# Performance work log

Measured on AMD Instinct MI355X. Metric: run time of the kernel, lower is better.

Reference implementation:

```python
import jax, jax.numpy as jnp
import numpy as np

NUM_ATOMS = 4_000_000
NUM_TYPES = 11

def setup_inputs() -> dict:
    key = jax.random.key(0)
    k1, k2 = jax.random.split(key)
    input_coords = jax.random.normal(k1, (3 * NUM_ATOMS,), dtype=jnp.float32)
    atom_types = jax.random.randint(k2, (NUM_ATOMS,), 0, NUM_TYPES, dtype=jnp.int64)
    return {"input_coords": input_coords, "atom_types": atom_types, "num_atom_types": NUM_TYPES}

def reference(input_coords, atom_types, num_atom_types):
    # counts per atom type  [T]
    counts = jnp.bincount(atom_types, length=num_atom_types).astype(jnp.int32)
    # exclusive prefix sum -> bucket offsets  [T]
    offsets = (jnp.cumsum(counts) - counts).astype(jnp.int32)
    # stable sort by type reproduces the C++ bucket fill order:
    # atoms of the same type keep their original relative order.
    perm = jnp.argsort(atom_types, stable=True)  # [N] source index for each output slot
    coords3 = input_coords.reshape(-1, 3)        # [N,3]
    typed_coords = coords3[perm].reshape(-1)     # [3N] type-grouped flat coords
    return typed_coords, counts, offsets
```

## Files before the change

kernel.cpp:

```cpp
#include <hip/hip_runtime.h>

#define NTYPES 11
#define BLOCK  256
#define ITEMS  16
#define CHUNK  (BLOCK * ITEMS)

__global__ __launch_bounds__(BLOCK) void hist_kernel(
    const int* __restrict__ types, int N, int B, int* __restrict__ bc) {
  __shared__ int shCnt[NTYPES];
  const int tid = threadIdx.x;
  const int b = blockIdx.x;
  if (tid < NTYPES) shCnt[tid] = 0;
  __syncthreads();

  const int run = b * CHUNK + tid * ITEMS;
  int cnt[NTYPES];
#pragma unroll
  for (int t = 0; t < NTYPES; ++t) cnt[t] = 0;

  if (run < N) {
    const int4* p = (const int4*)(types + run);
    int4 a0 = p[0], a1 = p[1], a2 = p[2], a3 = p[3];
    int ty[ITEMS] = {a0.x, a0.y, a0.z, a0.w, a1.x, a1.y, a1.z, a1.w,
                     a2.x, a2.y, a2.z, a2.w, a3.x, a3.y, a3.z, a3.w};
#pragma unroll
    for (int k = 0; k < ITEMS; ++k) {
#pragma unroll
      for (int t = 0; t < NTYPES; ++t) cnt[t] += (ty[k] == t) ? 1 : 0;
    }
  }

  const int lane = tid & 63;
#pragma unroll
  for (int t = 0; t < NTYPES; ++t) {
    int v = cnt[t];
    for (int o = 32; o >= 1; o >>= 1) v += __shfl_down(v, o);
    if (lane == 0) atomicAdd(&shCnt[t], v);
  }
  __syncthreads();
  if (tid < NTYPES) bc[tid * B + b] = shCnt[tid];
}

__global__ __launch_bounds__(1024) void scan_kernel(
    const int* __restrict__ bc, int B, int* __restrict__ scanOut,
    int* __restrict__ offs, float* __restrict__ outTail) {
  __shared__ int wtot[16];
  __shared__ int totals[NTYPES];
  const int tid = threadIdx.x;
  const int lane = tid & 63;
  const int wave = tid >> 6;

  for (int t = 0; t < NTYPES; ++t) {
    const int x = (tid < B) ? bc[t * B + tid] : 0;
    int incl = x;
#pragma unroll
    for (int o = 1; o < 64; o <<= 1) {
      int v = __shfl_up(incl, o);
      if (lane >= o) incl += v;
    }
    if (lane == 63) wtot[wave] = incl;
    __syncthreads();
    if (wave == 0) {
      int y = (lane < 16) ? wtot[lane] : 0;
#pragma unroll
      for (int o = 1; o < 16; o <<= 1) {
        int v = __shfl_up(y, o);
        if (lane >= o) y += v;
      }
      if (lane < 16) wtot[lane] = y;
    }
    __syncthreads();
    incl += (wave > 0) ? wtot[wave - 1] : 0;
    if (tid < B) scanOut[t * B + tid] = incl - x;
    if (tid == 1023) totals[t] = incl;
    __syncthreads();
  }

  if (tid == 0) {
    int off = 0;
    for (int t = 0; t < NTYPES; ++t) {
      const int c = totals[t];
      offs[t] = off;
      outTail[t] = (float)c;
      outTail[NTYPES + t] = (float)off;
      off += c;
    }
  }
}

__global__ __launch_bounds__(BLOCK) void scatter_kernel(
    const float* __restrict__ coords, const int* __restrict__ types,
    const int* __restrict__ scanOut, const int* __restrict__ offs, int N,
    int B, float* __restrict__ out) {
  const int tid = threadIdx.x;
  const int b = blockIdx.x;
  const int lane = tid & 63;
  const int wave = tid >> 6;
  const int run = b * CHUNK + tid * ITEMS;
  const bool active = (run < N);

  int ty[ITEMS];
  int cnt[NTYPES];
#pragma unroll
  for (int t = 0; t < NTYPES; ++t) cnt[t] = 0;
#pragma unroll
  for (int k = 0; k < ITEMS; ++k) ty[k] = -1;

  if (active) {
    const int4* p = (const int4*)(types + run);
    int4 a0 = p[0], a1 = p[1], a2 = p[2], a3 = p[3];
    int tt[ITEMS] = {a0.x, a0.y, a0.z, a0.w, a1.x, a1.y, a1.z, a1.w,
                     a2.x, a2.y, a2.z, a2.w, a3.x, a3.y, a3.z, a3.w};
#pragma unroll
    for (int k = 0; k < ITEMS; ++k) ty[k] = tt[k];
#pragma unroll
    for (int k = 0; k < ITEMS; ++k) {
#pragma unroll
      for (int t = 0; t < NTYPES; ++t) cnt[t] += (ty[k] == t) ? 1 : 0;
    }
  }

  __shared__ int wtot[NTYPES][4];
  int rank[NTYPES];
#pragma unroll
  for (int t = 0; t < NTYPES; ++t) {
    int incl = cnt[t];
#pragma unroll
    for (int o = 1; o < 64; o <<= 1) {
      int v = __shfl_up(incl, o);
      if (lane >= o) incl += v;
    }
    if (lane == 63) wtot[t][wave] = incl;
    rank[t] = incl - cnt[t];
  }
  __syncthreads();
#pragma unroll
  for (int t = 0; t < NTYPES; ++t) {
    int wb = 0;
#pragma unroll
    for (int w = 0; w < 3; ++w) wb += (w < wave) ? wtot[t][w] : 0;
    rank[t] += wb + offs[t] + scanOut[t * B + b];
  }

  if (active) {
    const float4* cp = (const float4*)(coords + (size_t)run * 3);
    float c[ITEMS * 3];
#pragma unroll
    for (int q = 0; q < 12; ++q) {
      float4 v = cp[q];
      c[4 * q + 0] = v.x;
      c[4 * q + 1] = v.y;
      c[4 * q + 2] = v.z;
      c[4 * q + 3] = v.w;
    }
#pragma unroll
    for (int k = 0; k < ITEMS; ++k) {
      const int t0 = ty[k];
      int dst = 0;
#pragma unroll
      for (int t = 0; t < NTYPES; ++t) {
        if (t0 == t) {
          dst = rank[t];
          rank[t] += 1;
        }
      }
      out[3 * (size_t)dst + 0] = c[3 * k + 0];
      out[3 * (size_t)dst + 1] = c[3 * k + 1];
      out[3 * (size_t)dst + 2] = c[3 * k + 2];
    }
  }
}

extern "C" void kernel_launch(void* const* d_in, const int* in_sizes, int n_in,
                              void* d_out, int out_size, void* d_ws,
                              size_t ws_size, hipStream_t stream) {
  const float* coords = (const float*)d_in[0];
  const int* types = (const int*)d_in[1];
  const int N = in_sizes[1];
  const int B = (N + CHUNK - 1) / CHUNK;

  int* bc = (int*)d_ws;
  int* scanOut = bc + NTYPES * B;
  int* offs = scanOut + NTYPES * B;
  float* out = (float*)d_out;
  float* outTail = out + (size_t)3 * N;

  hist_kernel<<<B, BLOCK, 0, stream>>>(types, N, B, bc);
  scan_kernel<<<1, 1024, 0, stream>>>(bc, B, scanOut, offs, outTail);
  scatter_kernel<<<B, BLOCK, 0, stream>>>(coords, types, scanOut, offs, N, B,
                                          out);
}
```

Measured before the change: 155.8 us.

## Stage scatter through shared memory so global writes are coalesced per bucket

The scatter kernel now ranks elements locally by type, writes their coordinates into a block-local shared buffer grouped by type, and then has consecutive threads copy consecutive slots to global memory with a per-type offset. This replaces the random per-thread scattered stores with mostly contiguous runs. The coordinate load is also moved earlier so it overlaps with the counting work. In exchange it uses about 48KB of LDS per block, which lowers occupancy, and it adds extra barriers.

```diff
diff --git a/kernel.cpp b/kernel.cpp
--- a/kernel.cpp
+++ b/kernel.cpp
@@ -92,6 +92,11 @@
     const float* __restrict__ coords, const int* __restrict__ types,
     const int* __restrict__ scanOut, const int* __restrict__ offs, int N,
     int B, float* __restrict__ out) {
+  __shared__ float shC[CHUNK * 3];
+  __shared__ int wtot[NTYPES][4];
+  __shared__ int shOff[NTYPES + 1];
+  __shared__ int shDelta[NTYPES];
+
   const int tid = threadIdx.x;
   const int b = blockIdx.x;
   const int lane = tid & 63;
@@ -106,6 +111,7 @@
 #pragma unroll
   for (int k = 0; k < ITEMS; ++k) ty[k] = -1;
 
+  float c[ITEMS * 3];
   if (active) {
     const int4* p = (const int4*)(types + run);
     int4 a0 = p[0], a1 = p[1], a2 = p[2], a3 = p[3];
@@ -113,38 +119,7 @@
                      a2.x, a2.y, a2.z, a2.w, a3.x, a3.y, a3.z, a3.w};
 #pragma unroll
     for (int k = 0; k < ITEMS; ++k) ty[k] = tt[k];
-#pragma unroll
-    for (int k = 0; k < ITEMS; ++k) {
-#pragma unroll
-      for (int t = 0; t < NTYPES; ++t) cnt[t] += (ty[k] == t) ? 1 : 0;
-    }
-  }
-
-  __shared__ int wtot[NTYPES][4];
-  int rank[NTYPES];
-#pragma unroll
-  for (int t = 0; t < NTYPES; ++t) {
-    int incl = cnt[t];
-#pragma unroll
-    for (int o = 1; o < 64; o <<= 1) {
-      int v = __shfl_up(incl, o);
-      if (lane >= o) incl += v;
-    }
-    if (lane == 63) wtot[t][wave] = incl;
-    rank[t] = incl - cnt[t];
-  }
-  __syncthreads();
-#pragma unroll
-  for (int t = 0; t < NTYPES; ++t) {
-    int wb = 0;
-#pragma unroll
-    for (int w = 0; w < 3; ++w) wb += (w < wave) ? wtot[t][w] : 0;
-    rank[t] += wb + offs[t] + scanOut[t * B + b];
-  }
-
-  if (active) {
     const float4* cp = (const float4*)(coords + (size_t)run * 3);
-    float c[ITEMS * 3];
 #pragma unroll
     for (int q = 0; q < 12; ++q) {
       float4 v = cp[q];
@@ -155,18 +130,84 @@
     }
 #pragma unroll
     for (int k = 0; k < ITEMS; ++k) {
+#pragma unroll
+      for (int t = 0; t < NTYPES; ++t) cnt[t] += (ty[k] == t) ? 1 : 0;
+    }
+  }
+
+  int rank[NTYPES];
+#pragma unroll
+  for (int t = 0; t < NTYPES; ++t) {
+    int incl = cnt[t];
+#pragma unroll
+    for (int o = 1; o < 64; o <<= 1) {
+      int v = __shfl_up(incl, o);
+      if (lane >= o) incl += v;
+    }
+    if (lane == 63) wtot[t][wave] = incl;
+    rank[t] = incl - cnt[t];
+  }
+  __syncthreads();
+
+  if (tid < NTYPES) {
+    int loc = 0;
+    for (int u = 0; u < tid; ++u)
+      loc += wtot[u][0] + wtot[u][1] + wtot[u][2] + wtot[u][3];
+    shOff[tid] = loc;
+    shDelta[tid] = 3 * (offs[tid] + scanOut[tid * B + b] - loc);
+    if (tid == NTYPES - 1) {
+      shOff[NTYPES] =
+          loc + wtot[tid][0] + wtot[tid][1] + wtot[tid][2] + wtot[tid][3];
+    }
+  }
+  __syncthreads();
+
+#pragma unroll
+  for (int t = 0; t < NTYPES; ++t) {
+    int wb = 0;
+#pragma unroll
+    for (int w = 0; w < 3; ++w) wb += (w < wave) ? wtot[t][w] : 0;
+    rank[t] += wb + shOff[t];
+  }
+
+  if (active) {
+#pragma unroll
+    for (int k = 0; k < ITEMS; ++k) {
       const int t0 = ty[k];
-      int dst = 0;
+      int slot = 0;
 #pragma unroll
       for (int t = 0; t < NTYPES; ++t) {
         if (t0 == t) {
-          dst = rank[t];
+          slot = rank[t];
           rank[t] += 1;
         }
       }
-      out[3 * (size_t)dst + 0] = c[3 * k + 0];
-      out[3 * (size_t)dst + 1] = c[3 * k + 1];
-      out[3 * (size_t)dst + 2] = c[3 * k + 2];
+      shC[3 * slot + 0] = c[3 * k + 0];
+      shC[3 * slot + 1] = c[3 * k + 1];
+      shC[3 * slot + 2] = c[3 * k + 2];
+    }
+  }
+  __syncthreads();
+
+  const int total = shOff[NTYPES];
+  int offr[NTYPES];
+  int dlt[NTYPES];
+#pragma unroll
+  for (int t = 0; t < NTYPES; ++t) {
+    offr[t] = shOff[t];
+    dlt[t] = shDelta[t];
+  }
+#pragma unroll
+  for (int k = 0; k < ITEMS; ++k) {
+    const int s = k * BLOCK + tid;
+    if (s < total) {
+      int d = dlt[0];
+#pragma unroll
+      for (int t = 1; t < NTYPES; ++t) d = (s >= offr[t]) ? dlt[t] : d;
+      const int src = 3 * s;
+      out[src + d + 0] = shC[src + 0];
+      out[src + d + 1] = shC[src + 1];
+      out[src + d + 2] = shC[src + 2];
     }
   }
 }
```

After: 140.2 us. 10.0% less time.
